# Kernel tuning notes

Hardware: AMD Instinct MI355X
Metric: run time of the kernel (lower is better)

Reference implementation:

```python
import jax, jax.numpy as jnp
import numpy as np

B, N, F_DIM, G_DIM, E_CAT, N_HEAD = 8, 1024, 128, 64, 2, 4
N_EDGES = 16384
L0 = 256          # NodeEmbedding hidden layer (layers=[256,128] -> last replaced by feature_size)
ALPHA = 0.5       # cfg.alpha
EPS = 1e-5        # BatchNorm eps
SLOPE = 0.01      # leaky_relu default negative slope


def _glorot(k, shape):
    stdv = float(np.sqrt(6.0 / (shape[-2] + shape[-1])))
    return jax.random.uniform(k, shape, jnp.float32, -stdv, stdv)


def setup_inputs() -> dict:
    key = jax.random.key(0)
    ks = jax.random.split(key, 8)
    X = jax.random.normal(ks[0], (B, N, F_DIM), dtype=jnp.float32)
    A = jax.random.randint(ks[1], (B, E_CAT, 2, N_EDGES), 0, N, dtype=jnp.int32)
    Ws = _glorot(ks[2], (E_CAT, N_HEAD * F_DIM, G_DIM))
    Wq = _glorot(ks[3], (E_CAT, N_HEAD * F_DIM, 1))
    Wv = _glorot(ks[4], (E_CAT, N_HEAD * F_DIM, 1))
    W_emb1 = _glorot(ks[5], (F_DIM, N_HEAD * E_CAT * G_DIM))   # Embedding1, bias=False
    W_lin0 = _glorot(ks[6], (L0, F_DIM))                        # NodeEmbedding linear0
    W_lin1 = _glorot(ks[7], (F_DIM, L0))                        # NodeEmbedding linear1
    return {"A": A, "X": X, "Ws": Ws, "Wq": Wq, "Wv": Wv,
            "W_emb1": W_emb1, "W_lin0": W_lin0, "W_lin1": W_lin1, "mini_batch": 1}


def _bn(x):
    # BatchNorm1d in training mode, affine = identity (weight=1, bias=0)
    mu = jnp.mean(x, axis=0)
    var = jnp.var(x, axis=0)  # biased variance, as torch uses for normalization
    return (x - mu) * jax.lax.rsqrt(var + EPS)


def _build_adj(A):
    # torch.sparse_coo_tensor(...).to_dense() sums duplicate edges
    adj = jnp.zeros((B, E_CAT, N, N), jnp.float32)
    b_idx = jnp.arange(B)[:, None, None]
    e_idx = jnp.arange(E_CAT)[None, :, None]
    return adj.at[b_idx, e_idx, A[:, :, 0], A[:, :, 1]].add(1.0)


def reference(A, X, Ws, Wq, Wv, W_emb1, W_lin0, W_lin1, mini_batch):
    Ws_r = Ws.reshape(E_CAT, N_HEAD, F_DIM, G_DIM)
    Wq_r = Wq.reshape(E_CAT, N_HEAD, F_DIM)   # last dim of Wq param is 1
    Wv_r = Wv.reshape(E_CAT, N_HEAD, F_DIM)

    Wh = jnp.einsum('bnf,ehfg->behng', X, Ws_r)   # [B,E,H,N,G]
    q = jnp.einsum('bnf,ehf->behn', X, Wq_r)      # [B,E,H,N]
    v = jnp.einsum('bnf,ehf->behn', X, Wv_r)

    adj = _build_adj(A)                            # [B,E,N,N]
    # e = (Wq @ Wv.T) * E, then leaky_relu and row softmax (dim=1 on [N,N] = last axis)
    scores = q[:, :, :, :, None] * v[:, :, :, None, :] * adj[:, :, None]
    scores = jnp.where(scores >= 0, scores, SLOPE * scores)
    a = jax.nn.softmax(scores, axis=-1)
    H = jnp.einsum('behnm,behmg->behng', a, Wh)    # [B,E,H,N,G]

    # concat over heads: [B,N, head-major (E*G)]
    H = H.transpose(0, 3, 2, 1, 4).reshape(B * N, N_HEAD * E_CAT * G_DIM)
    H = jax.nn.relu(H @ W_emb1.T)
    Xf = X.reshape(B * N, F_DIM)
    H = _bn((1.0 - ALPHA) * H + ALPHA * Xf)

    # NodeEmbedding: Linear -> BN -> ELU -> Linear
    Z = jax.nn.elu(_bn(H @ W_lin0.T))
    Z = Z @ W_lin1.T
    Z = _bn(H + Z)
    return Z.reshape(B, N, F_DIM)
```

## Files before the change

kernel.cpp:

```cpp
#include <hip/hip_runtime.h>
#include <hip/hip_bf16.h>

#define B_    8
#define N_    1024
#define F_    128
#define G_    64
#define EC    2
#define NHD   4
#define NE    16384
#define L0_   256
#define ALPHA_ 0.5f
#define EPS_   1e-5f
#define SLOPE_ 0.01f
#define ROWS  (B_*N_)
#define C1    (NHD*EC*G_)

__device__ __forceinline__ float ldv(const float* p, size_t i) { return p[i]; }
__device__ __forceinline__ float ldv(const __hip_bfloat16* p, size_t i) {
  unsigned short u = *(const unsigned short*)&p[i];
  return __uint_as_float((unsigned)u << 16);
}
__device__ __forceinline__ void ld4(const float* p, float& a, float& b, float& c, float& d) {
  float4 v = *(const float4*)p; a = v.x; b = v.y; c = v.z; d = v.w;
}
__device__ __forceinline__ void ld4(const __hip_bfloat16* p, float& a, float& b, float& c, float& d) {
  ushort4 v = *(const ushort4*)p;
  a = __uint_as_float((unsigned)v.x << 16); b = __uint_as_float((unsigned)v.y << 16);
  c = __uint_as_float((unsigned)v.z << 16); d = __uint_as_float((unsigned)v.w << 16);
}

__device__ __forceinline__ float wmaxf(float v) {
#pragma unroll
  for (int o = 32; o; o >>= 1) v = fmaxf(v, __shfl_xor(v, o, 64));
  return v;
}
__device__ __forceinline__ float wsumf(float v) {
#pragma unroll
  for (int o = 32; o; o >>= 1) v += __shfl_xor(v, o, 64);
  return v;
}

__global__ void k_detect(const unsigned short* Xu, int* flag) {
  int idx = blockIdx.x * 256 + threadIdx.x;
  unsigned short u = Xu[idx];
  if ((u & 0x7F80u) == 0x7F80u) atomicOr(flag, 1);
}

template <typename T>
__device__ __forceinline__ void proj_qv_body(const T* X, const T* Wq, const T* Wv,
                                             float* q, float* v) {
  int tid = threadIdx.x, lane = tid & 63, w = tid >> 6;
  int r = blockIdx.x * 4 + w;
  int n = r & (N_ - 1); int beh = r >> 10; int be = beh >> 2, h = beh & 3;
  int b = be >> 1, e = be & 1;
  const T* xr = X + ((size_t)(b * N_ + n)) * F_;
  const T* wq = Wq + (e * NHD + h) * F_;
  const T* wv = Wv + (e * NHD + h) * F_;
  float x0 = ldv(xr, lane), x1 = ldv(xr, lane + 64);
  float aq = x0 * ldv(wq, lane) + x1 * ldv(wq, lane + 64);
  float av = x0 * ldv(wv, lane) + x1 * ldv(wv, lane + 64);
  aq = wsumf(aq); av = wsumf(av);
  if (lane == 0) { q[r] = aq; v[r] = av; }
}
__global__ void k_proj_qv(const void* X, const void* Wq, const void* Wv,
                          float* q, float* v, const int* flag) {
  if (*flag) proj_qv_body<float>((const float*)X, (const float*)Wq, (const float*)Wv, q, v);
  else       proj_qv_body<__hip_bfloat16>((const __hip_bfloat16*)X, (const __hip_bfloat16*)Wq,
                                          (const __hip_bfloat16*)Wv, q, v);
}

template <typename TW>
__device__ __forceinline__ void wh_body(const TW* X, const TW* Wsrc, float* Wh, float* S,
                                        float* smem) {
  constexpr int KDIM = 128, KT = 64, NCOL = 64, RT = 64, RTP = 68, NP = 68;
  float* As = smem;
  float* Ws = smem + KT * RTP;
  int tid = threadIdx.x, tx = tid & 15, ty = tid >> 4;
  int row0 = blockIdx.x * RT; int eh = blockIdx.y;
  const TW* Wp = Wsrc + (size_t)eh * KDIM * NCOL;
  float acc[4][4] = {};
  for (int k0 = 0; k0 < KDIM; k0 += KT) {
    for (int t = tid; t < RT * KT / 4; t += 256) {
      int rr = t >> 4, k4 = t & 15;
      float a0, a1, a2, a3;
      ld4(X + (size_t)(row0 + rr) * KDIM + k0 + k4 * 4, a0, a1, a2, a3);
      As[(k4 * 4 + 0) * RTP + rr] = a0; As[(k4 * 4 + 1) * RTP + rr] = a1;
      As[(k4 * 4 + 2) * RTP + rr] = a2; As[(k4 * 4 + 3) * RTP + rr] = a3;
    }
    for (int t = tid; t < KT * NCOL / 4; t += 256) {
      int col4 = t & 15, k = t >> 4;
      float w0, w1, w2, w3;
      ld4(Wp + (size_t)(k0 + k) * NCOL + col4 * 4, w0, w1, w2, w3);
      *(float4*)(Ws + k * NP + col4 * 4) = make_float4(w0, w1, w2, w3);
    }
    __syncthreads();
#pragma unroll 4
    for (int k = 0; k < KT; ++k) {
      float4 av = *(const float4*)(As + k * RTP + ty * 4);
      float4 wv = *(const float4*)(Ws + k * NP + tx * 4);
      acc[0][0] += av.x * wv.x; acc[0][1] += av.x * wv.y; acc[0][2] += av.x * wv.z; acc[0][3] += av.x * wv.w;
      acc[1][0] += av.y * wv.x; acc[1][1] += av.y * wv.y; acc[1][2] += av.y * wv.z; acc[1][3] += av.y * wv.w;
      acc[2][0] += av.z * wv.x; acc[2][1] += av.z * wv.y; acc[2][2] += av.z * wv.z; acc[2][3] += av.z * wv.w;
      acc[3][0] += av.w * wv.x; acc[3][1] += av.w * wv.y; acc[3][2] += av.w * wv.z; acc[3][3] += av.w * wv.w;
    }
    __syncthreads();
  }
  int b = row0 >> 10;
  float colS[4] = {};
#pragma unroll
  for (int i = 0; i < 4; ++i) {
    int r = row0 + ty * 4 + i; int n = r & (N_ - 1);
    size_t base = ((size_t)(b * 8 + eh) * N_ + n) * G_ + tx * 4;
#pragma unroll
    for (int j = 0; j < 4; ++j) { Wh[base + j] = acc[i][j]; colS[j] += acc[i][j]; }
  }
  float* red = smem;
#pragma unroll
  for (int j = 0; j < 4; ++j) red[ty * 64 + tx * 4 + j] = colS[j];
  __syncthreads();
  if (tid < 64) {
    float s = 0.f;
#pragma unroll
    for (int t = 0; t < 16; ++t) s += red[t * 64 + tid];
    atomicAdd(&S[(size_t)(b * 8 + eh) * G_ + tid], s);
  }
}
__global__ __launch_bounds__(256) void k_whg(const void* X, const void* Ws, float* Wh,
                                             float* S, const int* flag) {
  __shared__ __align__(16) float smem[64 * 68 + 64 * 68];
  if (*flag) wh_body<float>((const float*)X, (const float*)Ws, Wh, S, smem);
  else       wh_body<__hip_bfloat16>((const __hip_bfloat16*)X, (const __hip_bfloat16*)Ws, Wh, S, smem);
}

__global__ void k_scatter2(const int* A, int* fill, int* colbuf) {
  int idx = blockIdx.x * 256 + threadIdx.x;
  int be = idx >> 14, i = idx & (NE - 1);
  int row = A[(size_t)(be * 2) * NE + i];
  int col = A[(size_t)(be * 2 + 1) * NE + i];
  int p = atomicAdd(&fill[be * N_ + row], 1);
  if (p < 64) colbuf[((size_t)(be * N_ + row)) * 64 + p] = col;
}

__global__ __launch_bounds__(256) void k_attn2(const float* q, const float* v, const float* Wh,
                                               const float* S, const int* fill,
                                               const int* colbuf, float* Hcat) {
  __shared__ int s_col[64];
  __shared__ int s_cnt[64];
  __shared__ int s_ld;
  __shared__ float s_w[4][64];
  int tid = threadIdx.x, lane = tid & 63, h = tid >> 6;
  int be = blockIdx.x >> 10, n = blockIdx.x & (N_ - 1);
  int b = be >> 1, e = be & 1;
  if (h == 0) {
    s_col[lane] = 0;
    int L = fill[be * N_ + n];
    int Lc = (L > 64) ? 64 : L;
    int myc = (lane < Lc) ? colbuf[((size_t)(be * N_ + n)) * 64 + lane] : -1;
    int cct = 0, firstk = 64;
    for (int k = 0; k < Lc; ++k) {
      int ck = __shfl(myc, k, 64);
      if (myc >= 0 && ck == myc) { cct++; if (k < firstk) firstk = k; }
    }
    bool act = (lane < Lc) && (firstk == lane);
    unsigned long long mask = __ballot(act);
    int pos = __popcll(mask & ((1ull << lane) - 1ull));
    if (act) { s_col[pos] = myc; s_cnt[pos] = cct; }
    if (lane == 0) s_ld = __popcll(mask);
  }
  __syncthreads();
  int Ld = s_ld;
  int beh = (be << 2) | h;
  float qn = q[beh * N_ + n];
  float sc = -1e30f;
  if (lane < Ld) {
    float t = qn * v[beh * N_ + s_col[lane]] * (float)s_cnt[lane];
    sc = (t >= 0.f) ? t : SLOPE_ * t;
  }
  float M = fmaxf(0.f, wmaxf(sc));
  float Ej = (lane < Ld) ? expf(sc - M) : 0.f;
  float sumE = wsumf(Ej);
  float em = expf(-M);
  float Z = (float)(N_ - Ld) * em + sumE;
  s_w[h][lane] = (lane < Ld) ? (Ej - em) / Z : 0.f;
  int eg = lane >> 4, g4 = (lane & 15) << 2;
  float4 accv = make_float4(0.f, 0.f, 0.f, 0.f);
  if (eg == 0) {
    float4 s4 = *(const float4*)&S[(size_t)beh * G_ + g4];
    float sca = em / Z;
    accv.x = sca * s4.x; accv.y = sca * s4.y; accv.z = sca * s4.z; accv.w = sca * s4.w;
  }
  const float* WhB = Wh + (size_t)beh * N_ * G_;
  for (int k0 = 0; k0 < Ld; k0 += 4) {
    int kk = k0 + eg;
    float wk = s_w[h][kk];
    int ck = s_col[kk];
    float4 x = *(const float4*)&WhB[(size_t)ck * G_ + g4];
    accv.x += wk * x.x; accv.y += wk * x.y; accv.z += wk * x.z; accv.w += wk * x.w;
  }
  accv.x += __shfl_xor(accv.x, 16, 64); accv.y += __shfl_xor(accv.y, 16, 64);
  accv.z += __shfl_xor(accv.z, 16, 64); accv.w += __shfl_xor(accv.w, 16, 64);
  accv.x += __shfl_xor(accv.x, 32, 64); accv.y += __shfl_xor(accv.y, 32, 64);
  accv.z += __shfl_xor(accv.z, 32, 64); accv.w += __shfl_xor(accv.w, 32, 64);
  if (lane < 16)
    *(float4*)&Hcat[((size_t)(b * N_ + n)) * C1 + h * (EC * G_) + e * G_ + g4] = accv;
}

template <int KDIM, int KT, int NCOL, int MODEA, int EP, typename TW>
__device__ __forceinline__ void gemm_body(
    const float* __restrict__ Araw, const TW* __restrict__ W, const TW* __restrict__ Xsrc,
    const float* __restrict__ Res,
    const float* sAsum, const float* sAssq, const float* sRsum, const float* sRssq,
    float* oSum, float* oSsq,
    float* __restrict__ C, int cstride, float* smem) {
  constexpr int RT = 32, RTP = 36, NP = NCOL + 4;
  float* As = smem;
  float* Ws = smem + KT * RTP;
  int tid = threadIdx.x, tx = tid & 15, ty = tid >> 4;
  int row0 = blockIdx.x * RT;
  int col0 = blockIdx.y * NCOL;
  float acc[2][4] = {};
  for (int k0 = 0; k0 < KDIM; k0 += KT) {
    for (int t = tid; t < RT * KT / 4; t += 256) {
      int rr = t / (KT / 4), k4 = t % (KT / 4);
      float4 val = *(const float4*)(Araw + (size_t)(row0 + rr) * KDIM + k0 + k4 * 4);
      if (MODEA) {
        float* vp = &val.x;
#pragma unroll
        for (int j = 0; j < 4; ++j) {
          int c = k0 + k4 * 4 + j;
          float mean = sAsum[c] * (1.f / ROWS);
          float var = sAssq[c] * (1.f / ROWS) - mean * mean;
          float y = (vp[j] - mean) * rsqrtf(var + EPS_);
          if (MODEA == 2) y = (y > 0.f) ? y : (expf(y) - 1.f);
          vp[j] = y;
        }
      }
      As[(k4 * 4 + 0) * RTP + rr] = val.x; As[(k4 * 4 + 1) * RTP + rr] = val.y;
      As[(k4 * 4 + 2) * RTP + rr] = val.z; As[(k4 * 4 + 3) * RTP + rr] = val.w;
    }
    for (int t = tid; t < NCOL * KT / 4; t += 256) {
      int col = t % NCOL, k4 = t / NCOL;
      float w0, w1, w2, w3;
      ld4(W + (size_t)(col0 + col) * KDIM + k0 + k4 * 4, w0, w1, w2, w3);
      Ws[(k4 * 4 + 0) * NP + col] = w0; Ws[(k4 * 4 + 1) * NP + col] = w1;
      Ws[(k4 * 4 + 2) * NP + col] = w2; Ws[(k4 * 4 + 3) * NP + col] = w3;
    }
    __syncthreads();
#pragma unroll 8
    for (int k = 0; k < KT; ++k) {
      float2 a2 = *(const float2*)(As + k * RTP + ty * 2);
      float4 wv = *(const float4*)(Ws + k * NP + tx * 4);
      acc[0][0] += a2.x * wv.x; acc[0][1] += a2.x * wv.y; acc[0][2] += a2.x * wv.z; acc[0][3] += a2.x * wv.w;
      acc[1][0] += a2.y * wv.x; acc[1][1] += a2.y * wv.y; acc[1][2] += a2.y * wv.z; acc[1][3] += a2.y * wv.w;
    }
    __syncthreads();
  }
  float colS[4] = {}, colS2[4] = {};
#pragma unroll
  for (int i = 0; i < 2; ++i) {
    int r = row0 + ty * 2 + i;
#pragma unroll
    for (int j = 0; j < 4; ++j) {
      int c = col0 + tx * 4 + j;
      float o = acc[i][j];
      if (EP == 1) {
        o = fmaxf(o, 0.f);
        o = (1.f - ALPHA_) * o + ALPHA_ * ldv(Xsrc, (size_t)r * F_ + c);
      } else if (EP == 2) {
        float x = Res[(size_t)r * 128 + c];
        float mean = sRsum[c] * (1.f / ROWS);
        float var = sRssq[c] * (1.f / ROWS) - mean * mean;
        o += (x - mean) * rsqrtf(var + EPS_);
      }
      C[(size_t)r * cstride + c] = o;
      colS[j] += o; colS2[j] += o * o;
    }
  }
  float* red = smem;
#pragma unroll
  for (int j = 0; j < 4; ++j) {
    red[ty * (NCOL * 2) + (tx * 4 + j) * 2 + 0] = colS[j];
    red[ty * (NCOL * 2) + (tx * 4 + j) * 2 + 1] = colS2[j];
  }
  __syncthreads();
  if (tid < NCOL) {
    float s = 0.f, s2 = 0.f;
#pragma unroll
    for (int t = 0; t < 16; ++t) {
      s += red[t * (NCOL * 2) + tid * 2]; s2 += red[t * (NCOL * 2) + tid * 2 + 1];
    }
    atomicAdd(&oSum[col0 + tid], s); atomicAdd(&oSsq[col0 + tid], s2);
  }
}

#define GEMM_SMEM (64 * 36 + 64 * 68)

__global__ __launch_bounds__(256) void k_mm1g(const float* A, const void* W, const void* X,
                                              float* C, float* oSum, float* oSsq,
                                              const int* flag) {
  __shared__ __align__(16) float smem[GEMM_SMEM];
  if (*flag)
    gemm_body<512, 64, 64, 0, 1, float>(A, (const float*)W, (const float*)X, nullptr,
                                        nullptr, nullptr, nullptr, nullptr, oSum, oSsq,
                                        C, 128, smem);
  else
    gemm_body<512, 64, 64, 0, 1, __hip_bfloat16>(A, (const __hip_bfloat16*)W,
                                                 (const __hip_bfloat16*)X, nullptr,
                                                 nullptr, nullptr, nullptr, nullptr, oSum, oSsq,
                                                 C, 128, smem);
}
__global__ __launch_bounds__(256) void k_lin0g(const float* A, const void* W, float* C,
                                               const float* s1sum, const float* s1ssq,
                                               float* oSum, float* oSsq, const int* flag) {
  __shared__ __align__(16) float smem[GEMM_SMEM];
  if (*flag)
    gemm_body<128, 64, 64, 1, 0, float>(A, (const float*)W, nullptr, nullptr,
                                        s1sum, s1ssq, nullptr, nullptr, oSum, oSsq,
                                        C, 256, smem);
  else
    gemm_body<128, 64, 64, 1, 0, __hip_bfloat16>(A, (const __hip_bfloat16*)W, nullptr, nullptr,
                                                 s1sum, s1ssq, nullptr, nullptr, oSum, oSsq,
                                                 C, 256, smem);
}
__global__ __launch_bounds__(256) void k_lin1g(const float* A, const void* W, const float* Res,
                                               float* C, const float* s2sum, const float* s2ssq,
                                               const float* s1sum, const float* s1ssq,
                                               float* oSum, float* oSsq, const int* flag) {
  __shared__ __align__(16) float smem[GEMM_SMEM];
  if (*flag)
    gemm_body<256, 64, 64, 2, 2, float>(A, (const float*)W, nullptr, Res,
                                        s2sum, s2ssq, s1sum, s1ssq, oSum, oSsq,
                                        C, 128, smem);
  else
    gemm_body<256, 64, 64, 2, 2, __hip_bfloat16>(A, (const __hip_bfloat16*)W, nullptr, Res,
                                                 s2sum, s2ssq, s1sum, s1ssq, oSum, oSsq,
                                                 C, 128, smem);
}

__global__ void k_norm_out(const float* in, void* out, const float* sum, const float* ssq,
                           const int* flag) {
  int idx = blockIdx.x * 256 + threadIdx.x; int c = idx & (F_ - 1);
  float mean = sum[c] * (1.f / ROWS);
  float var = ssq[c] * (1.f / ROWS) - mean * mean;
  float y = (in[idx] - mean) * rsqrtf(var + EPS_);
  if (*flag) ((float*)out)[idx] = y;
  else       ((__hip_bfloat16*)out)[idx] = __float2bfloat16(y);
}

extern "C" void kernel_launch(void* const* d_in, const int* in_sizes, int n_in,
                              void* d_out, int out_size, void* d_ws, size_t ws_size,
                              hipStream_t stream) {
  const int* A    = (const int*)d_in[0];
  const void* X   = d_in[1];
  const void* Ws  = d_in[2];
  const void* Wq  = d_in[3];
  const void* Wv  = d_in[4];
  const void* We1 = d_in[5];
  const void* Wl0 = d_in[6];
  const void* Wl1 = d_in[7];

  char* ws = (char*)d_ws;
  size_t off = 0;
  auto alloc = [&](size_t bytes) { size_t o = off; off += (bytes + 255) & ~(size_t)255; return o; };
  size_t o_fill   = alloc(16 * N_ * 4);
  size_t o_stats  = alloc(1024 * 4);
  size_t o_flag   = alloc(256);
  size_t o_S      = alloc((size_t)64 * G_ * 4);
  size_t zero_bytes = off;
  size_t o_colbuf = alloc((size_t)16 * N_ * 64 * 4);
  size_t o_q      = alloc((size_t)64 * N_ * 4);
  size_t o_v      = alloc((size_t)64 * N_ * 4);
  size_t o_Wh     = alloc((size_t)64 * N_ * G_ * 4);
  size_t o_Hcat   = alloc((size_t)ROWS * C1 * 4);
  size_t o_T4     = alloc((size_t)ROWS * F_ * 4);
  size_t o_T6     = alloc((size_t)ROWS * F_ * 4);
  size_t o_Z0     = alloc((size_t)ROWS * L0_ * 4);

  int*   fill   = (int*)(ws + o_fill);
  float* stats  = (float*)(ws + o_stats);
  int*   flag   = (int*)(ws + o_flag);
  float* S      = (float*)(ws + o_S);
  int*   colbuf = (int*)(ws + o_colbuf);
  float* q      = (float*)(ws + o_q);
  float* v      = (float*)(ws + o_v);
  float* Wh     = (float*)(ws + o_Wh);
  float* Hcat   = (float*)(ws + o_Hcat);
  float* T4     = (float*)(ws + o_T4);
  float* T6     = (float*)(ws + o_T6);
  float* Z0     = (float*)(ws + o_Z0);
  float* sum1 = stats,       *ssq1 = stats + 128;
  float* sum2 = stats + 256, *ssq2 = stats + 512;
  float* sum3 = stats + 768, *ssq3 = stats + 896;

  hipMemsetAsync(ws, 0, zero_bytes, stream);

  k_detect<<<512, 256, 0, stream>>>((const unsigned short*)X, flag);

  k_proj_qv<<<(64 * N_) / 4, 256, 0, stream>>>(X, Wq, Wv, q, v, flag);
  k_whg<<<dim3(ROWS / 64, 8), 256, 0, stream>>>(X, Ws, Wh, S, flag);

  k_scatter2<<<(16 * NE) / 256, 256, 0, stream>>>(A, fill, colbuf);

  k_attn2<<<16 * N_, 256, 0, stream>>>(q, v, Wh, S, fill, colbuf, Hcat);

  k_mm1g<<<dim3(ROWS / 32, 2), 256, 0, stream>>>(Hcat, We1, X, T4, sum1, ssq1, flag);
  k_lin0g<<<dim3(ROWS / 32, 4), 256, 0, stream>>>(T4, Wl0, Z0, sum1, ssq1, sum2, ssq2, flag);
  k_lin1g<<<dim3(ROWS / 32, 2), 256, 0, stream>>>(Z0, Wl1, T4, T6, sum2, ssq2, sum1, ssq1,
                                                  sum3, ssq3, flag);
  k_norm_out<<<(ROWS * F_) / 256, 256, 0, stream>>>(T6, d_out, sum3, ssq3, flag);

  (void)in_sizes; (void)n_in; (void)out_size; (void)ws_size;
}
```

Measured before the change: 249.6 us.

## Replace fp32 LDS GEMMs with bf16 MFMA kernels and fold BN into lin0 weights

Converts X and the weights to bf16 up front, then runs all four dense GEMMs (Wh, Embedding1, lin0, lin1) as one-wavefront MFMA 16x16x32 bf16 kernels that read operands straight from global memory. The attention output and intermediates are stored in bf16 to halve traffic. The first BatchNorm is folded into the lin0 weights plus a bias, and ELU+BN gets its own elementwise pass. This targets the FP32 FMA and LDS-bound GEMM cost, at the price of bf16 rounding error, extra conversion and elementwise kernels, and more launches.

```diff
diff --git a/kernel.cpp b/kernel.cpp
--- a/kernel.cpp
+++ b/kernel.cpp
@@ -15,18 +15,21 @@
 #define ROWS  (B_*N_)
 #define C1    (NHD*EC*G_)
 
+typedef __attribute__((ext_vector_type(8))) short s8bf;
+typedef __attribute__((ext_vector_type(4))) float f32x4;
+
 __device__ __forceinline__ float ldv(const float* p, size_t i) { return p[i]; }
 __device__ __forceinline__ float ldv(const __hip_bfloat16* p, size_t i) {
   unsigned short u = *(const unsigned short*)&p[i];
   return __uint_as_float((unsigned)u << 16);
 }
-__device__ __forceinline__ void ld4(const float* p, float& a, float& b, float& c, float& d) {
-  float4 v = *(const float4*)p; a = v.x; b = v.y; c = v.z; d = v.w;
-}
-__device__ __forceinline__ void ld4(const __hip_bfloat16* p, float& a, float& b, float& c, float& d) {
-  ushort4 v = *(const ushort4*)p;
-  a = __uint_as_float((unsigned)v.x << 16); b = __uint_as_float((unsigned)v.y << 16);
-  c = __uint_as_float((unsigned)v.z << 16); d = __uint_as_float((unsigned)v.w << 16);
+__device__ __forceinline__ unsigned short f2b(float f) {
+  unsigned u = __float_as_uint(f);
+  u = (u + 0x7FFFu + ((u >> 16) & 1u)) >> 16;
+  return (unsigned short)u;
+}
+__device__ __forceinline__ float b2f(unsigned short u) {
+  return __uint_as_float((unsigned)u << 16);
 }
 
 __device__ __forceinline__ float wmaxf(float v) {
@@ -44,6 +47,28 @@
   int idx = blockIdx.x * 256 + threadIdx.x;
   unsigned short u = Xu[idx];
   if ((u & 0x7F80u) == 0x7F80u) atomicOr(flag, 1);
+}
+
+__device__ __forceinline__ unsigned short cvt_at(const void* p, size_t i, int isf) {
+  return isf ? f2b(((const float*)p)[i]) : ((const unsigned short*)p)[i];
+}
+__global__ void k_cvtw(const void* X, const void* Ws, const void* We1, const void* Wl1,
+                       unsigned short* Xb, unsigned short* Wsb, unsigned short* We1b,
+                       unsigned short* Wl1b, const int* flag) {
+  int isf = *flag;
+  int bid = blockIdx.x, t = threadIdx.x;
+  if (bid < 4096) {
+    int i = bid * 256 + t; Xb[i] = cvt_at(X, i, isf);
+  } else if (bid < 4352) {
+    int i = (bid - 4096) * 256 + t; We1b[i] = cvt_at(We1, i, isf);
+  } else if (bid < 4480) {
+    int i = (bid - 4352) * 256 + t; Wl1b[i] = cvt_at(Wl1, i, isf);
+  } else {
+    int i = (bid - 4480) * 256 + t;
+    int eh = i >> 13, rem = i & 8191;
+    int g = rem >> 7, f = rem & 127;
+    Wsb[eh * 8192 + g * 128 + f] = cvt_at(Ws, (size_t)eh * 8192 + f * 64 + g, isf);
+  }
 }
 
 template <typename T>
@@ -69,67 +94,49 @@
                                           (const __hip_bfloat16*)Wv, q, v);
 }
 
-template <typename TW>
-__device__ __forceinline__ void wh_body(const TW* X, const TW* Wsrc, float* Wh, float* S,
-                                        float* smem) {
-  constexpr int KDIM = 128, KT = 64, NCOL = 64, RT = 64, RTP = 68, NP = 68;
-  float* As = smem;
-  float* Ws = smem + KT * RTP;
-  int tid = threadIdx.x, tx = tid & 15, ty = tid >> 4;
-  int row0 = blockIdx.x * RT; int eh = blockIdx.y;
-  const TW* Wp = Wsrc + (size_t)eh * KDIM * NCOL;
-  float acc[4][4] = {};
-  for (int k0 = 0; k0 < KDIM; k0 += KT) {
-    for (int t = tid; t < RT * KT / 4; t += 256) {
-      int rr = t >> 4, k4 = t & 15;
-      float a0, a1, a2, a3;
-      ld4(X + (size_t)(row0 + rr) * KDIM + k0 + k4 * 4, a0, a1, a2, a3);
-      As[(k4 * 4 + 0) * RTP + rr] = a0; As[(k4 * 4 + 1) * RTP + rr] = a1;
-      As[(k4 * 4 + 2) * RTP + rr] = a2; As[(k4 * 4 + 3) * RTP + rr] = a3;
-    }
-    for (int t = tid; t < KT * NCOL / 4; t += 256) {
-      int col4 = t & 15, k = t >> 4;
-      float w0, w1, w2, w3;
-      ld4(Wp + (size_t)(k0 + k) * NCOL + col4 * 4, w0, w1, w2, w3);
-      *(float4*)(Ws + k * NP + col4 * 4) = make_float4(w0, w1, w2, w3);
-    }
-    __syncthreads();
-#pragma unroll 4
-    for (int k = 0; k < KT; ++k) {
-      float4 av = *(const float4*)(As + k * RTP + ty * 4);
-      float4 wv = *(const float4*)(Ws + k * NP + tx * 4);
-      acc[0][0] += av.x * wv.x; acc[0][1] += av.x * wv.y; acc[0][2] += av.x * wv.z; acc[0][3] += av.x * wv.w;
-      acc[1][0] += av.y * wv.x; acc[1][1] += av.y * wv.y; acc[1][2] += av.y * wv.z; acc[1][3] += av.y * wv.w;
-      acc[2][0] += av.z * wv.x; acc[2][1] += av.z * wv.y; acc[2][2] += av.z * wv.z; acc[2][3] += av.z * wv.w;
-      acc[3][0] += av.w * wv.x; acc[3][1] += av.w * wv.y; acc[3][2] += av.w * wv.z; acc[3][3] += av.w * wv.w;
-    }
-    __syncthreads();
-  }
-  int b = row0 >> 10;
-  float colS[4] = {};
-#pragma unroll
-  for (int i = 0; i < 4; ++i) {
-    int r = row0 + ty * 4 + i; int n = r & (N_ - 1);
-    size_t base = ((size_t)(b * 8 + eh) * N_ + n) * G_ + tx * 4;
-#pragma unroll
-    for (int j = 0; j < 4; ++j) { Wh[base + j] = acc[i][j]; colS[j] += acc[i][j]; }
-  }
-  float* red = smem;
-#pragma unroll
-  for (int j = 0; j < 4; ++j) red[ty * 64 + tx * 4 + j] = colS[j];
-  __syncthreads();
-  if (tid < 64) {
+template <int K>
+__device__ __forceinline__ void mfma_core(const unsigned short* __restrict__ Ab,
+                                          const unsigned short* __restrict__ Wb,
+                                          int r0, int c0, f32x4* acc) {
+  int lane = threadIdx.x & 63; int q = lane >> 4, c15 = lane & 15;
+  constexpr int RS = K / 8;
+  const s8bf* ap = (const s8bf*)Ab + (size_t)(r0 + c15) * RS + q;
+  const s8bf* bp = (const s8bf*)Wb + (size_t)(c0 + c15) * RS + q;
+#pragma unroll
+  for (int ks = 0; ks < K / 32; ++ks) {
+    s8bf a  = ap[ks * 4];
+    s8bf b0 = bp[ks * 4];
+    s8bf b1 = bp[16 * RS + ks * 4];
+    s8bf b2 = bp[32 * RS + ks * 4];
+    s8bf b3 = bp[48 * RS + ks * 4];
+    acc[0] = __builtin_amdgcn_mfma_f32_16x16x32_bf16(a, b0, acc[0], 0, 0, 0);
+    acc[1] = __builtin_amdgcn_mfma_f32_16x16x32_bf16(a, b1, acc[1], 0, 0, 0);
+    acc[2] = __builtin_amdgcn_mfma_f32_16x16x32_bf16(a, b2, acc[2], 0, 0, 0);
+    acc[3] = __builtin_amdgcn_mfma_f32_16x16x32_bf16(a, b3, acc[3], 0, 0, 0);
+  }
+}
+
+__global__ __launch_bounds__(64) void k_whm(const unsigned short* Xb,
+                                            const unsigned short* Wsb,
+                                            float* Wh, float* S) {
+  int r0 = blockIdx.x * 16; int eh = blockIdx.y;
+  f32x4 acc[4] = {{0,0,0,0},{0,0,0,0},{0,0,0,0},{0,0,0,0}};
+  mfma_core<128>(Xb, Wsb + eh * 8192, r0, 0, acc);
+  int lane = threadIdx.x, q = lane >> 4, c15 = lane & 15;
+  int b = r0 >> 10; int beh = b * 8 + eh;
+  float* WhB = Wh + ((size_t)beh * N_ + (r0 & (N_ - 1))) * G_;
+#pragma unroll
+  for (int nc = 0; nc < 4; ++nc) {
     float s = 0.f;
 #pragma unroll
-    for (int t = 0; t < 16; ++t) s += red[t * 64 + tid];
-    atomicAdd(&S[(size_t)(b * 8 + eh) * G_ + tid], s);
-  }
-}
-__global__ __launch_bounds__(256) void k_whg(const void* X, const void* Ws, float* Wh,
-                                             float* S, const int* flag) {
-  __shared__ __align__(16) float smem[64 * 68 + 64 * 68];
-  if (*flag) wh_body<float>((const float*)X, (const float*)Ws, Wh, S, smem);
-  else       wh_body<__hip_bfloat16>((const __hip_bfloat16*)X, (const __hip_bfloat16*)Ws, Wh, S, smem);
+    for (int i = 0; i < 4; ++i) {
+      float o = acc[nc][i];
+      WhB[(size_t)(q * 4 + i) * G_ + nc * 16 + c15] = o;
+      s += o;
+    }
+    s += __shfl_xor(s, 16, 64); s += __shfl_xor(s, 32, 64);
+    if (lane < 16) atomicAdd(&S[(size_t)beh * G_ + nc * 16 + lane], s);
+  }
 }
 
 __global__ void k_scatter2(const int* A, int* fill, int* colbuf) {
@@ -143,7 +150,7 @@
 
 __global__ __launch_bounds__(256) void k_attn2(const float* q, const float* v, const float* Wh,
                                                const float* S, const int* fill,
-                                               const int* colbuf, float* Hcat) {
+                                               const int* colbuf, unsigned short* Hcatb) {
   __shared__ int s_col[64];
   __shared__ int s_cnt[64];
   __shared__ int s_ld;
@@ -201,140 +208,136 @@
   accv.z += __shfl_xor(accv.z, 16, 64); accv.w += __shfl_xor(accv.w, 16, 64);
   accv.x += __shfl_xor(accv.x, 32, 64); accv.y += __shfl_xor(accv.y, 32, 64);
   accv.z += __shfl_xor(accv.z, 32, 64); accv.w += __shfl_xor(accv.w, 32, 64);
-  if (lane < 16)
-    *(float4*)&Hcat[((size_t)(b * N_ + n)) * C1 + h * (EC * G_) + e * G_ + g4] = accv;
-}
-
-template <int KDIM, int KT, int NCOL, int MODEA, int EP, typename TW>
-__device__ __forceinline__ void gemm_body(
-    const float* __restrict__ Araw, const TW* __restrict__ W, const TW* __restrict__ Xsrc,
-    const float* __restrict__ Res,
-    const float* sAsum, const float* sAssq, const float* sRsum, const float* sRssq,
-    float* oSum, float* oSsq,
-    float* __restrict__ C, int cstride, float* smem) {
-  constexpr int RT = 32, RTP = 36, NP = NCOL + 4;
-  float* As = smem;
-  float* Ws = smem + KT * RTP;
-  int tid = threadIdx.x, tx = tid & 15, ty = tid >> 4;
-  int row0 = blockIdx.x * RT;
-  int col0 = blockIdx.y * NCOL;
-  float acc[2][4] = {};
-  for (int k0 = 0; k0 < KDIM; k0 += KT) {
-    for (int t = tid; t < RT * KT / 4; t += 256) {
-      int rr = t / (KT / 4), k4 = t % (KT / 4);
-      float4 val = *(const float4*)(Araw + (size_t)(row0 + rr) * KDIM + k0 + k4 * 4);
-      if (MODEA) {
-        float* vp = &val.x;
-#pragma unroll
-        for (int j = 0; j < 4; ++j) {
-          int c = k0 + k4 * 4 + j;
-          float mean = sAsum[c] * (1.f / ROWS);
-          float var = sAssq[c] * (1.f / ROWS) - mean * mean;
-          float y = (vp[j] - mean) * rsqrtf(var + EPS_);
-          if (MODEA == 2) y = (y > 0.f) ? y : (expf(y) - 1.f);
-          vp[j] = y;
-        }
-      }
-      As[(k4 * 4 + 0) * RTP + rr] = val.x; As[(k4 * 4 + 1) * RTP + rr] = val.y;
-      As[(k4 * 4 + 2) * RTP + rr] = val.z; As[(k4 * 4 + 3) * RTP + rr] = val.w;
-    }
-    for (int t = tid; t < NCOL * KT / 4; t += 256) {
-      int col = t % NCOL, k4 = t / NCOL;
-      float w0, w1, w2, w3;
-      ld4(W + (size_t)(col0 + col) * KDIM + k0 + k4 * 4, w0, w1, w2, w3);
-      Ws[(k4 * 4 + 0) * NP + col] = w0; Ws[(k4 * 4 + 1) * NP + col] = w1;
-      Ws[(k4 * 4 + 2) * NP + col] = w2; Ws[(k4 * 4 + 3) * NP + col] = w3;
-    }
-    __syncthreads();
-#pragma unroll 8
-    for (int k = 0; k < KT; ++k) {
-      float2 a2 = *(const float2*)(As + k * RTP + ty * 2);
-      float4 wv = *(const float4*)(Ws + k * NP + tx * 4);
-      acc[0][0] += a2.x * wv.x; acc[0][1] += a2.x * wv.y; acc[0][2] += a2.x * wv.z; acc[0][3] += a2.x * wv.w;
-      acc[1][0] += a2.y * wv.x; acc[1][1] += a2.y * wv.y; acc[1][2] += a2.y * wv.z; acc[1][3] += a2.y * wv.w;
-    }
-    __syncthreads();
-  }
-  float colS[4] = {}, colS2[4] = {};
-#pragma unroll
-  for (int i = 0; i < 2; ++i) {
-    int r = row0 + ty * 2 + i;
-#pragma unroll
-    for (int j = 0; j < 4; ++j) {
-      int c = col0 + tx * 4 + j;
-      float o = acc[i][j];
-      if (EP == 1) {
-        o = fmaxf(o, 0.f);
-        o = (1.f - ALPHA_) * o + ALPHA_ * ldv(Xsrc, (size_t)r * F_ + c);
-      } else if (EP == 2) {
-        float x = Res[(size_t)r * 128 + c];
-        float mean = sRsum[c] * (1.f / ROWS);
-        float var = sRssq[c] * (1.f / ROWS) - mean * mean;
-        o += (x - mean) * rsqrtf(var + EPS_);
-      }
-      C[(size_t)r * cstride + c] = o;
-      colS[j] += o; colS2[j] += o * o;
-    }
-  }
-  float* red = smem;
-#pragma unroll
-  for (int j = 0; j < 4; ++j) {
-    red[ty * (NCOL * 2) + (tx * 4 + j) * 2 + 0] = colS[j];
-    red[ty * (NCOL * 2) + (tx * 4 + j) * 2 + 1] = colS2[j];
-  }
+  if (lane < 16) {
+    ushort4 o;
+    o.x = f2b(accv.x); o.y = f2b(accv.y); o.z = f2b(accv.z); o.w = f2b(accv.w);
+    *(ushort4*)&Hcatb[((size_t)(b * N_ + n)) * C1 + h * (EC * G_) + e * G_ + g4] = o;
+  }
+}
+
+template <typename TX>
+__device__ __forceinline__ void mm1_ep(f32x4* acc, const TX* X, float* T4,
+                                       unsigned short* T4b, float* sum1, float* ssq1,
+                                       int r0, int c0) {
+  int lane = threadIdx.x, q = lane >> 4, c15 = lane & 15;
+#pragma unroll
+  for (int nc = 0; nc < 4; ++nc) {
+    int cc = c0 + nc * 16 + c15;
+    float s = 0.f, s2 = 0.f;
+#pragma unroll
+    for (int i = 0; i < 4; ++i) {
+      int rr = r0 + q * 4 + i;
+      float o = fmaxf(acc[nc][i], 0.f);
+      o = 0.5f * o + 0.5f * ldv(X, (size_t)rr * F_ + cc);
+      T4[(size_t)rr * F_ + cc] = o;
+      T4b[(size_t)rr * F_ + cc] = f2b(o);
+      s += o; s2 += o * o;
+    }
+    s += __shfl_xor(s, 16, 64); s += __shfl_xor(s, 32, 64);
+    s2 += __shfl_xor(s2, 16, 64); s2 += __shfl_xor(s2, 32, 64);
+    if (lane < 16) {
+      atomicAdd(&sum1[c0 + nc * 16 + lane], s);
+      atomicAdd(&ssq1[c0 + nc * 16 + lane], s2);
+    }
+  }
+}
+__global__ __launch_bounds__(64) void k_mm1m(const unsigned short* Hcatb,
+                                             const unsigned short* We1b, const void* X,
+                                             float* T4, unsigned short* T4b,
+                                             float* sum1, float* ssq1, const int* flag) {
+  int r0 = blockIdx.x * 16, c0 = blockIdx.y * 64;
+  f32x4 acc[4] = {{0,0,0,0},{0,0,0,0},{0,0,0,0},{0,0,0,0}};
+  mfma_core<512>(Hcatb, We1b, r0, c0, acc);
+  if (*flag) mm1_ep<float>(acc, (const float*)X, T4, T4b, sum1, ssq1, r0, c0);
+  else       mm1_ep<__hip_bfloat16>(acc, (const __hip_bfloat16*)X, T4, T4b, sum1, ssq1, r0, c0);
+}
+
+__global__ void k_fold0(const void* Wl0, const float* sum1, const float* ssq1,
+                        unsigned short* W0p, float* bias0, const int* flag) {
+  __shared__ float red[2];
+  int c = blockIdx.x, k = threadIdx.x;
+  float mean = sum1[k] * (1.f / ROWS);
+  float var = ssq1[k] * (1.f / ROWS) - mean * mean;
+  float rs = rsqrtf(var + EPS_);
+  float w = (*flag) ? ((const float*)Wl0)[(size_t)c * F_ + k]
+                    : b2f(((const unsigned short*)Wl0)[(size_t)c * F_ + k]);
+  unsigned short wb = f2b(w * rs);
+  W0p[(size_t)c * F_ + k] = wb;
+  float part = mean * b2f(wb);
+  part = wsumf(part);
+  if ((threadIdx.x & 63) == 0) red[threadIdx.x >> 6] = part;
   __syncthreads();
-  if (tid < NCOL) {
+  if (threadIdx.x == 0) bias0[c] = red[0] + red[1];
+}
+
+__global__ __launch_bounds__(64) void k_lin0m(const unsigned short* T4b,
+                                              const unsigned short* W0p, const float* bias0,
+                                              float* Z0, float* sum2, float* ssq2) {
+  int r0 = blockIdx.x * 16, c0 = blockIdx.y * 64;
+  f32x4 acc[4] = {{0,0,0,0},{0,0,0,0},{0,0,0,0},{0,0,0,0}};
+  mfma_core<128>(T4b, W0p, r0, c0, acc);
+  int lane = threadIdx.x, q = lane >> 4, c15 = lane & 15;
+#pragma unroll
+  for (int nc = 0; nc < 4; ++nc) {
+    int cc = c0 + nc * 16 + c15;
+    float bia = bias0[cc];
     float s = 0.f, s2 = 0.f;
 #pragma unroll
-    for (int t = 0; t < 16; ++t) {
-      s += red[t * (NCOL * 2) + tid * 2]; s2 += red[t * (NCOL * 2) + tid * 2 + 1];
-    }
-    atomicAdd(&oSum[col0 + tid], s); atomicAdd(&oSsq[col0 + tid], s2);
-  }
-}
-
-#define GEMM_SMEM (64 * 36 + 64 * 68)
-
-__global__ __launch_bounds__(256) void k_mm1g(const float* A, const void* W, const void* X,
-                                              float* C, float* oSum, float* oSsq,
-                                              const int* flag) {
-  __shared__ __align__(16) float smem[GEMM_SMEM];
-  if (*flag)
-    gemm_body<512, 64, 64, 0, 1, float>(A, (const float*)W, (const float*)X, nullptr,
-                                        nullptr, nullptr, nullptr, nullptr, oSum, oSsq,
-                                        C, 128, smem);
-  else
-    gemm_body<512, 64, 64, 0, 1, __hip_bfloat16>(A, (const __hip_bfloat16*)W,
-                                                 (const __hip_bfloat16*)X, nullptr,
-                                                 nullptr, nullptr, nullptr, nullptr, oSum, oSsq,
-                                                 C, 128, smem);
-}
-__global__ __launch_bounds__(256) void k_lin0g(const float* A, const void* W, float* C,
-                                               const float* s1sum, const float* s1ssq,
-                                               float* oSum, float* oSsq, const int* flag) {
-  __shared__ __align__(16) float smem[GEMM_SMEM];
-  if (*flag)
-    gemm_body<128, 64, 64, 1, 0, float>(A, (const float*)W, nullptr, nullptr,
-                                        s1sum, s1ssq, nullptr, nullptr, oSum, oSsq,
-                                        C, 256, smem);
-  else
-    gemm_body<128, 64, 64, 1, 0, __hip_bfloat16>(A, (const __hip_bfloat16*)W, nullptr, nullptr,
-                                                 s1sum, s1ssq, nullptr, nullptr, oSum, oSsq,
-                                                 C, 256, smem);
-}
-__global__ __launch_bounds__(256) void k_lin1g(const float* A, const void* W, const float* Res,
-                                               float* C, const float* s2sum, const float* s2ssq,
-                                               const float* s1sum, const float* s1ssq,
-                                               float* oSum, float* oSsq, const int* flag) {
-  __shared__ __align__(16) float smem[GEMM_SMEM];
-  if (*flag)
-    gemm_body<256, 64, 64, 2, 2, float>(A, (const float*)W, nullptr, Res,
-                                        s2sum, s2ssq, s1sum, s1ssq, oSum, oSsq,
-                                        C, 128, smem);
-  else
-    gemm_body<256, 64, 64, 2, 2, __hip_bfloat16>(A, (const __hip_bfloat16*)W, nullptr, Res,
-                                                 s2sum, s2ssq, s1sum, s1ssq, oSum, oSsq,
-                                                 C, 128, smem);
+    for (int i = 0; i < 4; ++i) {
+      int rr = r0 + q * 4 + i;
+      float o = acc[nc][i] - bia;
+      Z0[(size_t)rr * L0_ + cc] = o;
+      s += o; s2 += o * o;
+    }
+    s += __shfl_xor(s, 16, 64); s += __shfl_xor(s, 32, 64);
+    s2 += __shfl_xor(s2, 16, 64); s2 += __shfl_xor(s2, 32, 64);
+    if (lane < 16) {
+      atomicAdd(&sum2[c0 + nc * 16 + lane], s);
+      atomicAdd(&ssq2[c0 + nc * 16 + lane], s2);
+    }
+  }
+}
+
+__global__ void k_elu(const float* Z0, unsigned short* E, const float* sum2,
+                      const float* ssq2) {
+  int idx = blockIdx.x * 256 + threadIdx.x;
+  int c = idx & (L0_ - 1);
+  float mean = sum2[c] * (1.f / ROWS);
+  float var = ssq2[c] * (1.f / ROWS) - mean * mean;
+  float y = (Z0[idx] - mean) * rsqrtf(var + EPS_);
+  y = (y > 0.f) ? y : (expf(y) - 1.f);
+  E[idx] = f2b(y);
+}
+
+__global__ __launch_bounds__(64) void k_lin1m(const unsigned short* E,
+                                              const unsigned short* Wl1b, const float* T4,
+                                              const float* sum1, const float* ssq1,
+                                              float* T6, float* sum3, float* ssq3) {
+  int r0 = blockIdx.x * 16, c0 = blockIdx.y * 64;
+  f32x4 acc[4] = {{0,0,0,0},{0,0,0,0},{0,0,0,0},{0,0,0,0}};
+  mfma_core<256>(E, Wl1b, r0, c0, acc);
+  int lane = threadIdx.x, q = lane >> 4, c15 = lane & 15;
+#pragma unroll
+  for (int nc = 0; nc < 4; ++nc) {
+    int cc = c0 + nc * 16 + c15;
+    float mean = sum1[cc] * (1.f / ROWS);
+    float var = ssq1[cc] * (1.f / ROWS) - mean * mean;
+    float rs = rsqrtf(var + EPS_);
+    float s = 0.f, s2 = 0.f;
+#pragma unroll
+    for (int i = 0; i < 4; ++i) {
+      int rr = r0 + q * 4 + i;
+      float o = acc[nc][i] + (T4[(size_t)rr * F_ + cc] - mean) * rs;
+      T6[(size_t)rr * F_ + cc] = o;
+      s += o; s2 += o * o;
+    }
+    s += __shfl_xor(s, 16, 64); s += __shfl_xor(s, 32, 64);
+    s2 += __shfl_xor(s2, 16, 64); s2 += __shfl_xor(s2, 32, 64);
+    if (lane < 16) {
+      atomicAdd(&sum3[c0 + nc * 16 + lane], s);
+      atomicAdd(&ssq3[c0 + nc * 16 + lane], s2);
+    }
+  }
 }
 
 __global__ void k_norm_out(const float* in, void* out, const float* sum, const float* ssq,
@@ -371,10 +374,18 @@
   size_t o_q      = alloc((size_t)64 * N_ * 4);
   size_t o_v      = alloc((size_t)64 * N_ * 4);
   size_t o_Wh     = alloc((size_t)64 * N_ * G_ * 4);
-  size_t o_Hcat   = alloc((size_t)ROWS * C1 * 4);
+  size_t o_Hcatb  = alloc((size_t)ROWS * C1 * 2);
   size_t o_T4     = alloc((size_t)ROWS * F_ * 4);
+  size_t o_T4b    = alloc((size_t)ROWS * F_ * 2);
   size_t o_T6     = alloc((size_t)ROWS * F_ * 4);
   size_t o_Z0     = alloc((size_t)ROWS * L0_ * 4);
+  size_t o_E      = alloc((size_t)ROWS * L0_ * 2);
+  size_t o_Xb     = alloc((size_t)ROWS * F_ * 2);
+  size_t o_Wsb    = alloc((size_t)8 * G_ * F_ * 2);
+  size_t o_We1b   = alloc((size_t)F_ * C1 * 2);
+  size_t o_Wl1b   = alloc((size_t)F_ * L0_ * 2);
+  size_t o_W0p    = alloc((size_t)L0_ * F_ * 2);
+  size_t o_bias0  = alloc(L0_ * 4);
 
   int*   fill   = (int*)(ws + o_fill);
   float* stats  = (float*)(ws + o_stats);
@@ -384,10 +395,18 @@
   float* q      = (float*)(ws + o_q);
   float* v      = (float*)(ws + o_v);
   float* Wh     = (float*)(ws + o_Wh);
-  float* Hcat   = (float*)(ws + o_Hcat);
+  unsigned short* Hcatb = (unsigned short*)(ws + o_Hcatb);
   float* T4     = (float*)(ws + o_T4);
+  unsigned short* T4b   = (unsigned short*)(ws + o_T4b);
   float* T6     = (float*)(ws + o_T6);
   float* Z0     = (float*)(ws + o_Z0);
+  unsigned short* E     = (unsigned short*)(ws + o_E);
+  unsigned short* Xb    = (unsigned short*)(ws + o_Xb);
+  unsigned short* Wsb   = (unsigned short*)(ws + o_Wsb);
+  unsigned short* We1b  = (unsigned short*)(ws + o_We1b);
+  unsigned short* Wl1b  = (unsigned short*)(ws + o_Wl1b);
+  unsigned short* W0p   = (unsigned short*)(ws + o_W0p);
+  float* bias0  = (float*)(ws + o_bias0);
   float* sum1 = stats,       *ssq1 = stats + 128;
   float* sum2 = stats + 256, *ssq2 = stats + 512;
   float* sum3 = stats + 768, *ssq3 = stats + 896;
@@ -395,18 +414,19 @@
   hipMemsetAsync(ws, 0, zero_bytes, stream);
 
   k_detect<<<512, 256, 0, stream>>>((const unsigned short*)X, flag);
+  k_cvtw<<<4736, 256, 0, stream>>>(X, Ws, We1, Wl1, Xb, Wsb, We1b, Wl1b, flag);
 
   k_proj_qv<<<(64 * N_) / 4, 256, 0, stream>>>(X, Wq, Wv, q, v, flag);
-  k_whg<<<dim3(ROWS / 64, 8), 256, 0, stream>>>(X, Ws, Wh, S, flag);
+  k_whm<<<dim3(ROWS / 16, 8), 64, 0, stream>>>(Xb, Wsb, Wh, S);
 
   k_scatter2<<<(16 * NE) / 256, 256, 0, stream>>>(A, fill, colbuf);
-
-  k_attn2<<<16 * N_, 256, 0, stream>>>(q, v, Wh, S, fill, colbuf, Hcat);
-
-  k_mm1g<<<dim3(ROWS / 32, 2), 256, 0, stream>>>(Hcat, We1, X, T4, sum1, ssq1, flag);
-  k_lin0g<<<dim3(ROWS / 32, 4), 256, 0, stream>>>(T4, Wl0, Z0, sum1, ssq1, sum2, ssq2, flag);
-  k_lin1g<<<dim3(ROWS / 32, 2), 256, 0, stream>>>(Z0, Wl1, T4, T6, sum2, ssq2, sum1, ssq1,
-                                                  sum3, ssq3, flag);
+  k_attn2<<<16 * N_, 256, 0, stream>>>(q, v, Wh, S, fill, colbuf, Hcatb);
+
+  k_mm1m<<<dim3(ROWS / 16, 2), 64, 0, stream>>>(Hcatb, We1b, X, T4, T4b, sum1, ssq1, flag);
+  k_fold0<<<L0_, 128, 0, stream>>>(Wl0, sum1, ssq1, W0p, bias0, flag);
+  k_lin0m<<<dim3(ROWS / 16, 4), 64, 0, stream>>>(T4b, W0p, bias0, Z0, sum2, ssq2);
+  k_elu<<<(ROWS * L0_) / 256, 256, 0, stream>>>(Z0, E, sum2, ssq2);
+  k_lin1m<<<dim3(ROWS / 16, 2), 64, 0, stream>>>(E, Wl1b, T4, sum1, ssq1, T6, sum3, ssq3);
   k_norm_out<<<(ROWS * F_) / 256, 256, 0, stream>>>(T6, d_out, sum3, ssq3, flag);
 
   (void)in_sizes; (void)n_in; (void)out_size; (void)ws_size;
```

New measurement: 247.3 us. No clear change (-0.9%).
